# Performance work log

Measured on AMD Instinct MI355X. Metric: run time of the kernel, lower is better.

## Reference

```python
import jax, jax.numpy as jnp
import numpy as np

B, T, D, R = 4, 2048, 1024, 64  # batch, seq_len, hidden_dim, max_relative_position


def setup_inputs() -> dict:
    key = jax.random.key(0)
    ks = jax.random.split(key, 11)
    s = 1.0 / np.sqrt(D)

    def lin(k):
        return (jax.random.normal(k, (D, D), jnp.float32) * s)

    return {
        "repre": jax.random.normal(ks[0], (B, T, D), jnp.float32),
        "mask": jnp.ones((B, T, T), jnp.int32),  # 1 = valid position
        "st_Wq": lin(ks[1]), "st_bq": jnp.zeros((D,), jnp.float32),
        "st_Wk": lin(ks[2]), "st_bk": jnp.zeros((D,), jnp.float32),
        "st_rel": jax.random.normal(ks[3], (2 * R + 1, D), jnp.float32) * 0.02,
        "ed_Wq": lin(ks[4]), "ed_bq": jnp.zeros((D,), jnp.float32),
        "ed_Wk": lin(ks[5]), "ed_bk": jnp.zeros((D,), jnp.float32),
        "ed_rel": jax.random.normal(ks[6], (2 * R + 1, D), jnp.float32) * 0.02,
    }


def _attn_logits(x, Wq, bq, Wk, bk, rel, mask):
    # Single-head attention scores with relative-position key bias (OpenNMT style).
    d = x.shape[-1]
    q = (x @ Wq + bq) * (1.0 / jnp.sqrt(jnp.float32(d)))  # [B,T,D], pre-scaled query
    k = x @ Wk + bk                                        # [B,T,D]
    scores = jnp.einsum('btd,bsd->bts', q, k)              # [B,T,T] content scores
    Tn = x.shape[1]
    Rn = (rel.shape[0] - 1) // 2
    pos = jnp.arange(Tn)
    # relative position matrix: clip(j - i, -R, R) + R  -> [T,T] indices
    idx = jnp.clip(pos[None, :] - pos[:, None], -Rn, Rn) + Rn
    # q . rel_emb for every relative offset, then gather per (i,j):
    # equivalent to einsum('btd,tsd->bts', q, rel[idx]) without the [T,T,D] gather.
    qr = jnp.einsum('btd,rd->btr', q, rel)                 # [B,T,2R+1]
    scores = scores + qr[:, pos[:, None], idx]             # [B,T,T]
    return jnp.where(mask.astype(bool), scores, jnp.float32(-1e18))


def reference(repre, mask, st_Wq, st_bq, st_Wk, st_bk, st_rel,
              ed_Wq, ed_bq, ed_Wk, ed_bk, ed_rel):
    span_st_logits = _attn_logits(repre, st_Wq, st_bq, st_Wk, st_bk, st_rel, mask)
    span_ed_logits = _attn_logits(repre, ed_Wq, ed_bq, ed_Wk, ed_bk, ed_rel, mask)
    return (span_st_logits, span_ed_logits)
```

## Files before the change

kernel.cpp:

```cpp
#include <hip/hip_runtime.h>

constexpr int Bn = 4;
constexpr int Tn = 2048;
constexpr int Dn = 1024;
constexpr int Rn = 64;
constexpr int RELP = 256;
constexpr int QR_STRIDE = 132;

typedef __bf16 bf8 __attribute__((ext_vector_type(8)));
typedef float f32x4 __attribute__((ext_vector_type(4)));

__device__ __forceinline__ unsigned short f2bf(float f) {
    unsigned int u = __float_as_uint(f);
    u += 0x7fffu + ((u >> 16) & 1u);
    return (unsigned short)(u >> 16);
}

#define GLDS(g, l)                                                            \
    __builtin_amdgcn_global_load_lds(                                         \
        (const __attribute__((address_space(1))) void*)(g),                   \
        (__attribute__((address_space(3))) void*)(l), 16, 0, 0)

__device__ __forceinline__ void mfma_gemm_128(
    const unsigned short* __restrict__ Ab,
    const unsigned short* __restrict__ Bb,
    int K, f32x4 acc[4][4],
    unsigned short* As, unsigned short* Bs)
{
    const int tid = threadIdx.x;
    const int r0  = tid >> 2;
    const int c8  = (tid & 3) * 8;
    const int lane = tid & 63;
    const int w    = tid >> 6;
    const int wm = (w & 1) * 64, wn = (w >> 1) * 64;
    const int l15 = lane & 15, lq = lane >> 4;

    const int nt = K >> 5;

    GLDS(Ab + (size_t)r0 * K + c8,        As + r0 * 32 + c8);
    GLDS(Ab + ((size_t)r0 + 64) * K + c8, As + (r0 + 64) * 32 + c8);
    GLDS(Bb + (size_t)r0 * K + c8,        Bs + r0 * 32 + c8);
    GLDS(Bb + ((size_t)r0 + 64) * K + c8, Bs + (r0 + 64) * 32 + c8);
    __syncthreads();

    int cur = 0;
    for (int t = 0; t < nt; ++t) {
        if (t + 1 < nt) {
            const int k0 = (t + 1) << 5;
            const int nb = (cur ^ 1) * (128 * 32);
            GLDS(Ab + (size_t)r0 * K + k0 + c8,        As + nb + r0 * 32 + c8);
            GLDS(Ab + ((size_t)r0 + 64) * K + k0 + c8, As + nb + (r0 + 64) * 32 + c8);
            GLDS(Bb + (size_t)r0 * K + k0 + c8,        Bs + nb + r0 * 32 + c8);
            GLDS(Bb + ((size_t)r0 + 64) * K + k0 + c8, Bs + nb + (r0 + 64) * 32 + c8);
        }
        const int cb = cur * (128 * 32);
        bf8 a[4], b[4];
#pragma unroll
        for (int i = 0; i < 4; ++i) {
            a[i] = *(const bf8*)&As[cb + (wm + i * 16 + l15) * 32 + lq * 8];
            b[i] = *(const bf8*)&Bs[cb + (wn + i * 16 + l15) * 32 + lq * 8];
        }
#pragma unroll
        for (int i = 0; i < 4; ++i)
#pragma unroll
            for (int j = 0; j < 4; ++j)
                acc[i][j] = __builtin_amdgcn_mfma_f32_16x16x32_bf16(
                    a[i], b[j], acc[i][j], 0, 0, 0);
        __syncthreads();
        cur ^= 1;
    }
}

__global__ __launch_bounds__(256) void cvt_bf16(
    const float* __restrict__ in, unsigned short* __restrict__ out, int n4)
{
    int i = blockIdx.x * 256 + threadIdx.x;
    if (i < n4) {
        float4 v = ((const float4*)in)[i];
        ushort4 o;
        o.x = f2bf(v.x); o.y = f2bf(v.y); o.z = f2bf(v.z); o.w = f2bf(v.w);
        ((ushort4*)out)[i] = o;
    }
}

__global__ __launch_bounds__(256) void wt_transpose(
    const float* __restrict__ w0, const float* __restrict__ w1,
    const float* __restrict__ w2, const float* __restrict__ w3,
    unsigned short* __restrict__ WT)
{
    __shared__ float t[32][33];
    const int z = blockIdx.z;
    const float* W = z == 0 ? w0 : z == 1 ? w1 : z == 2 ? w2 : w3;
    const int x = blockIdx.x * 32 + threadIdx.x;
    const int y0 = blockIdx.y * 32;
#pragma unroll
    for (int j = 0; j < 32; j += 8)
        t[threadIdx.y + j][threadIdx.x] = W[(size_t)(y0 + threadIdx.y + j) * Dn + x];
    __syncthreads();
    unsigned short* o = WT + (size_t)z * Dn * Dn;
    const int n0 = blockIdx.x * 32;
#pragma unroll
    for (int j = 0; j < 32; j += 8)
        o[(size_t)(n0 + threadIdx.y + j) * Dn + y0 + threadIdx.x] =
            f2bf(t[threadIdx.x][threadIdx.y + j]);
}

__global__ __launch_bounds__(256) void rel_pad(
    const float* __restrict__ st_rel, const float* __restrict__ ed_rel,
    unsigned short* __restrict__ relb)
{
    const int z = blockIdx.y;
    const float* in = z ? ed_rel : st_rel;
    const int i4 = blockIdx.x * 256 + threadIdx.x;
    const int row = (i4 * 4) >> 10;
    const int col = (i4 * 4) & 1023;
    ushort4 o; o.x = 0; o.y = 0; o.z = 0; o.w = 0;
    if (row < 2 * Rn + 1) {
        float4 v = *(const float4*)(in + (size_t)row * 1024 + col);
        o.x = f2bf(v.x); o.y = f2bf(v.y); o.z = f2bf(v.z); o.w = f2bf(v.w);
    }
    ((ushort4*)(relb + (size_t)z * RELP * 1024))[i4] = o;
}

__global__ __launch_bounds__(256) void proj_gemm(
    const unsigned short* __restrict__ Xb, const unsigned short* __restrict__ Wb,
    const float* __restrict__ b0, const float* __restrict__ b1,
    const float* __restrict__ b2, const float* __restrict__ b3,
    unsigned short* __restrict__ outQK, float qscale)
{
    __shared__ unsigned short As[2 * 128 * 32], Bs[2 * 128 * 32];
    const int z = blockIdx.z;
    const float* bias = z == 0 ? b0 : z == 1 ? b1 : z == 2 ? b2 : b3;
    const float scale = (z & 1) ? 1.0f : qscale;

    const unsigned short* Ab = Xb + (size_t)blockIdx.x * 128 * Dn;
    const unsigned short* Bb = Wb + ((size_t)z * Dn + blockIdx.y * 128) * Dn;

    f32x4 zero = {0.f, 0.f, 0.f, 0.f};
    f32x4 acc[4][4];
#pragma unroll
    for (int i = 0; i < 4; ++i)
#pragma unroll
        for (int j = 0; j < 4; ++j) acc[i][j] = zero;

    mfma_gemm_128(Ab, Bb, Dn, acc, As, Bs);

    const int tid = threadIdx.x, lane = tid & 63, w = tid >> 6;
    const int wm = (w & 1) * 64, wn = (w >> 1) * 64;
    const int l15 = lane & 15, lq = lane >> 4;
    unsigned short* out = outQK + (size_t)z * (size_t)Bn * Tn * Dn;

#pragma unroll
    for (int ni = 0; ni < 4; ++ni) {
        const int col = blockIdx.y * 128 + wn + ni * 16 + l15;
        const float bv = bias[col];
#pragma unroll
        for (int mi = 0; mi < 4; ++mi) {
#pragma unroll
            for (int r = 0; r < 4; ++r) {
                const int row = blockIdx.x * 128 + wm + mi * 16 + lq * 4 + r;
                out[(size_t)row * Dn + col] = f2bf((acc[mi][ni][r] + bv) * scale);
            }
        }
    }
}

__global__ __launch_bounds__(256) void qr_gemm(
    const unsigned short* __restrict__ QKb, const unsigned short* __restrict__ relb,
    float* __restrict__ QR)
{
    __shared__ unsigned short As[2 * 128 * 32], Bs[2 * 128 * 32];
    const int z = blockIdx.z;
    const unsigned short* Ab = QKb + ((size_t)(z * 2) * Bn * Tn + blockIdx.x * 128) * Dn;
    const unsigned short* Bb = relb + ((size_t)z * RELP + blockIdx.y * 128) * Dn;

    f32x4 zero = {0.f, 0.f, 0.f, 0.f};
    f32x4 acc[4][4];
#pragma unroll
    for (int i = 0; i < 4; ++i)
#pragma unroll
        for (int j = 0; j < 4; ++j) acc[i][j] = zero;

    mfma_gemm_128(Ab, Bb, Dn, acc, As, Bs);

    const int tid = threadIdx.x, lane = tid & 63, w = tid >> 6;
    const int wm = (w & 1) * 64, wn = (w >> 1) * 64;
    const int l15 = lane & 15, lq = lane >> 4;
    float* out = QR + (size_t)z * (size_t)Bn * Tn * QR_STRIDE;

#pragma unroll
    for (int ni = 0; ni < 4; ++ni) {
        const int col = blockIdx.y * 128 + wn + ni * 16 + l15;
        if (col >= 2 * Rn + 1) continue;
#pragma unroll
        for (int mi = 0; mi < 4; ++mi) {
#pragma unroll
            for (int r = 0; r < 4; ++r) {
                const int row = blockIdx.x * 128 + wm + mi * 16 + lq * 4 + r;
                out[(size_t)row * QR_STRIDE + col] = acc[mi][ni][r];
            }
        }
    }
}

__global__ __launch_bounds__(256) void scores_gemm(
    const unsigned short* __restrict__ QKb, const float* __restrict__ QR,
    const int* __restrict__ mask, float* __restrict__ Out)
{
    __shared__ unsigned short As[2 * 128 * 32], Bs[2 * 128 * 32];
    const int z = blockIdx.z;
    const int side = z >> 2, bt = z & 3;

    const unsigned short* Ab =
        QKb + ((size_t)side * 2 * Bn * Tn + (size_t)bt * Tn + blockIdx.x * 128) * Dn;
    const unsigned short* Bb =
        QKb + (((size_t)side * 2 + 1) * Bn * Tn + (size_t)bt * Tn + blockIdx.y * 128) * Dn;
    const float* QRb = QR + ((size_t)side * Bn * Tn + (size_t)bt * Tn) * QR_STRIDE;
    const int* maskb = mask + (size_t)bt * Tn * Tn;
    float* outb = Out + ((size_t)side * Bn + bt) * (size_t)Tn * Tn;

    f32x4 zero = {0.f, 0.f, 0.f, 0.f};
    f32x4 acc[4][4];
#pragma unroll
    for (int i = 0; i < 4; ++i)
#pragma unroll
        for (int j = 0; j < 4; ++j) acc[i][j] = zero;

    mfma_gemm_128(Ab, Bb, Dn, acc, As, Bs);

    const int tid = threadIdx.x, lane = tid & 63, w = tid >> 6;
    const int wm = (w & 1) * 64, wn = (w >> 1) * 64;
    const int l15 = lane & 15, lq = lane >> 4;

#pragma unroll
    for (int mi = 0; mi < 4; ++mi) {
#pragma unroll
        for (int r = 0; r < 4; ++r) {
            const int i = blockIdx.x * 128 + wm + mi * 16 + lq * 4 + r;
            const float* qrow = QRb + (size_t)i * QR_STRIDE;
            const int* mrow = maskb + (size_t)i * Tn;
            float* orow = outb + (size_t)i * Tn;
#pragma unroll
            for (int ni = 0; ni < 4; ++ni) {
                const int j = blockIdx.y * 128 + wn + ni * 16 + l15;
                int d = j - i;
                d = d < -Rn ? -Rn : (d > Rn ? Rn : d);
                const float qv = qrow[d + Rn];
                orow[j] = mrow[j] ? acc[mi][ni][r] + qv : -1e18f;
            }
        }
    }
}

extern "C" void kernel_launch(void* const* d_in, const int* in_sizes, int n_in,
                              void* d_out, int out_size, void* d_ws, size_t ws_size,
                              hipStream_t stream) {
    const float* repre  = (const float*)d_in[0];
    const int*   mask   = (const int*)  d_in[1];
    const float* st_Wq  = (const float*)d_in[2];
    const float* st_bq  = (const float*)d_in[3];
    const float* st_Wk  = (const float*)d_in[4];
    const float* st_bk  = (const float*)d_in[5];
    const float* st_rel = (const float*)d_in[6];
    const float* ed_Wq  = (const float*)d_in[7];
    const float* ed_bq  = (const float*)d_in[8];
    const float* ed_Wk  = (const float*)d_in[9];
    const float* ed_bk  = (const float*)d_in[10];
    const float* ed_rel = (const float*)d_in[11];
    float* out = (float*)d_out;

    const size_t MT = (size_t)Bn * Tn;

    unsigned short* Xb   = (unsigned short*)d_ws;
    unsigned short* Wb   = Xb + MT * Dn;
    unsigned short* relb = Wb + (size_t)4 * Dn * Dn;
    unsigned short* QKb  = relb + (size_t)2 * RELP * Dn;
    float* QRbuf = (float*)(QKb + (size_t)4 * MT * Dn);

    const float qscale = 0.03125f;
    dim3 blk(256);

    {
        int n4 = (int)(MT * Dn / 4);
        cvt_bf16<<<dim3((n4 + 255) / 256), blk, 0, stream>>>(repre, Xb, n4);
        wt_transpose<<<dim3(32, 32, 4), dim3(32, 8), 0, stream>>>(
            st_Wq, st_Wk, ed_Wq, ed_Wk, Wb);
        rel_pad<<<dim3(RELP * Dn / 4 / 256, 2), blk, 0, stream>>>(st_rel, ed_rel, relb);
    }

    proj_gemm<<<dim3((int)MT / 128, Dn / 128, 4), blk, 0, stream>>>(
        Xb, Wb, st_bq, st_bk, ed_bq, ed_bk, QKb, qscale);

    qr_gemm<<<dim3((int)MT / 128, RELP / 128, 2), blk, 0, stream>>>(QKb, relb, QRbuf);

    scores_gemm<<<dim3(Tn / 128, Tn / 128, 8), blk, 0, stream>>>(QKb, QRbuf, mask, out);
}
```

Before: 557.8 us.

## Use 256x256 tiles with triple-buffered swizzled LDS pipeline for proj and score GEMMs

Replaces the 128x128 double-buffered GEMM core with a 256x256 tile per 512-thread block, an XOR-swizzled LDS layout, three-stage global_load_lds prefetch, and split MFMA phases under raised wave priority. Both the projection GEMM and the score GEMM now use it. The larger tiles cut global and LDS traffic per FLOP and the deeper pipeline is meant to hide load latency. The cost is more registers and LDS per block, fewer blocks in each grid, and hand-tuned waitcnt and barrier logic.

```diff
diff --git a/kernel.cpp b/kernel.cpp
--- a/kernel.cpp
+++ b/kernel.cpp
@@ -20,6 +20,100 @@
     __builtin_amdgcn_global_load_lds(                                         \
         (const __attribute__((address_space(1))) void*)(g),                   \
         (__attribute__((address_space(3))) void*)(l), 16, 0, 0)
+
+#define MFMA_BF16(a, b, c) __builtin_amdgcn_mfma_f32_16x16x32_bf16(a, b, c, 0, 0, 0)
+
+#define SBAR()                                                                \
+    do {                                                                      \
+        __builtin_amdgcn_sched_barrier(0);                                    \
+        __builtin_amdgcn_s_barrier();                                         \
+    } while (0)
+
+__device__ __forceinline__ void mfma_gemm_256_k32(
+    const unsigned short* __restrict__ Ab,
+    const unsigned short* __restrict__ Bb,
+    f32x4 (&acc)[8][4], unsigned short* As, unsigned short* Bs)
+{
+    const int tid  = threadIdx.x;
+    const int lane = tid & 63, wid = tid >> 6;
+    const int wr = wid >> 2, wc = wid & 3;
+    const int l15 = lane & 15, lq = lane >> 4;
+
+    const int pc = (((l15 & 1) << 2) | lq) ^ ((l15 >> 1) & 7);
+    const int lane_off = ((l15 >> 1) << 6) + (pc << 3);
+    const int aoff = wr * 4096 + lane_off;
+    const int boff = wc * 2048 + lane_off;
+
+    const int P0 = tid, P1 = tid + 512;
+    const int cr0 = P0 >> 3, cr1 = P1 >> 3;
+    const int c0 = cr0 * 8 + ((P0 & 7) ^ (cr0 & 7));
+    const int c1 = cr1 * 8 + ((P1 & 7) ^ (cr1 & 7));
+    const size_t g0 = (size_t)(c0 >> 2) * Dn + (size_t)((c0 & 3) << 3);
+    const size_t g1 = (size_t)(c1 >> 2) * Dn + (size_t)((c1 & 3) << 3);
+    const int d0 = P0 * 8, d1 = P1 * 8;
+
+#define STAGE(src, buf)                                                       \
+    do {                                                                      \
+        GLDS((src) + g0, (buf) + d0);                                         \
+        GLDS((src) + g1, (buf) + d1);                                         \
+    } while (0)
+
+    constexpr int NT = Dn / 32;
+
+    STAGE(Ab, As);
+    STAGE(Bb, Bs);
+    STAGE(Ab + 32, As + 8192);
+    STAGE(Bb + 32, Bs + 8192);
+    asm volatile("s_waitcnt vmcnt(4)" ::: "memory");
+    SBAR();
+
+    int bufi = 0;
+    bf8 a8[8], b4[4];
+#pragma unroll 1
+    for (int T = 0; T < NT; ++T) {
+        const int cb  = bufi << 13;
+        const int sb  = (bufi == 0 ? 2 : bufi - 1) << 13;
+        const bool st = T < NT - 2;
+        const unsigned short* At = Ab + (T + 2) * 32;
+        const unsigned short* Bt = Bb + (T + 2) * 32;
+
+#pragma unroll
+        for (int m = 0; m < 8; ++m)
+            a8[m] = *(const bf8*)&As[cb + aoff + m * 512];
+        b4[0] = *(const bf8*)&Bs[cb + boff];
+        b4[1] = *(const bf8*)&Bs[cb + boff + 512];
+        if (st) STAGE(At, As + sb);
+        SBAR();
+        __builtin_amdgcn_s_setprio(1);
+#pragma unroll
+        for (int m = 0; m < 8; ++m) {
+            acc[m][0] = MFMA_BF16(a8[m], b4[0], acc[m][0]);
+            acc[m][1] = MFMA_BF16(a8[m], b4[1], acc[m][1]);
+        }
+        __builtin_amdgcn_s_setprio(0);
+        SBAR();
+
+        b4[2] = *(const bf8*)&Bs[cb + boff + 1024];
+        b4[3] = *(const bf8*)&Bs[cb + boff + 1536];
+        if (st) STAGE(Bt, Bs + sb);
+        SBAR();
+        __builtin_amdgcn_s_setprio(1);
+#pragma unroll
+        for (int m = 0; m < 8; ++m) {
+            acc[m][2] = MFMA_BF16(a8[m], b4[2], acc[m][2]);
+            acc[m][3] = MFMA_BF16(a8[m], b4[3], acc[m][3]);
+        }
+        __builtin_amdgcn_s_setprio(0);
+        if (st) {
+            asm volatile("s_waitcnt vmcnt(4)" ::: "memory");
+        } else if (T == NT - 2) {
+            asm volatile("s_waitcnt vmcnt(0)" ::: "memory");
+        }
+        if (T < NT - 1) SBAR();
+        bufi = (bufi == 2) ? 0 : bufi + 1;
+    }
+#undef STAGE
+}
 
 __device__ __forceinline__ void mfma_gemm_128(
     const unsigned short* __restrict__ Ab,
@@ -53,19 +147,18 @@
             GLDS(Bb + (size_t)r0 * K + k0 + c8,        Bs + nb + r0 * 32 + c8);
             GLDS(Bb + ((size_t)r0 + 64) * K + k0 + c8, Bs + nb + (r0 + 64) * 32 + c8);
         }
-        const int cb = cur * (128 * 32);
+        const int cbuf = cur * (128 * 32);
         bf8 a[4], b[4];
 #pragma unroll
         for (int i = 0; i < 4; ++i) {
-            a[i] = *(const bf8*)&As[cb + (wm + i * 16 + l15) * 32 + lq * 8];
-            b[i] = *(const bf8*)&Bs[cb + (wn + i * 16 + l15) * 32 + lq * 8];
+            a[i] = *(const bf8*)&As[cbuf + (wm + i * 16 + l15) * 32 + lq * 8];
+            b[i] = *(const bf8*)&Bs[cbuf + (wn + i * 16 + l15) * 32 + lq * 8];
         }
 #pragma unroll
         for (int i = 0; i < 4; ++i)
 #pragma unroll
             for (int j = 0; j < 4; ++j)
-                acc[i][j] = __builtin_amdgcn_mfma_f32_16x16x32_bf16(
-                    a[i], b[j], acc[i][j], 0, 0, 0);
+                acc[i][j] = MFMA_BF16(a[i], b[j], acc[i][j]);
         __syncthreads();
         cur ^= 1;
     }
@@ -122,46 +215,47 @@
     ((ushort4*)(relb + (size_t)z * RELP * 1024))[i4] = o;
 }
 
-__global__ __launch_bounds__(256) void proj_gemm(
+__global__ __launch_bounds__(512, 2) void proj_gemm256(
     const unsigned short* __restrict__ Xb, const unsigned short* __restrict__ Wb,
     const float* __restrict__ b0, const float* __restrict__ b1,
     const float* __restrict__ b2, const float* __restrict__ b3,
     unsigned short* __restrict__ outQK, float qscale)
 {
-    __shared__ unsigned short As[2 * 128 * 32], Bs[2 * 128 * 32];
+    __shared__ unsigned short As[3 * 8192], Bs[3 * 8192];
     const int z = blockIdx.z;
     const float* bias = z == 0 ? b0 : z == 1 ? b1 : z == 2 ? b2 : b3;
     const float scale = (z & 1) ? 1.0f : qscale;
 
-    const unsigned short* Ab = Xb + (size_t)blockIdx.x * 128 * Dn;
-    const unsigned short* Bb = Wb + ((size_t)z * Dn + blockIdx.y * 128) * Dn;
+    const unsigned short* Ab = Xb + (size_t)blockIdx.x * 256 * Dn;
+    const unsigned short* Bb = Wb + ((size_t)z * Dn + blockIdx.y * 256) * Dn;
 
     f32x4 zero = {0.f, 0.f, 0.f, 0.f};
-    f32x4 acc[4][4];
-#pragma unroll
-    for (int i = 0; i < 4; ++i)
+    f32x4 acc[8][4];
+#pragma unroll
+    for (int i = 0; i < 8; ++i)
 #pragma unroll
         for (int j = 0; j < 4; ++j) acc[i][j] = zero;
 
-    mfma_gemm_128(Ab, Bb, Dn, acc, As, Bs);
-
-    const int tid = threadIdx.x, lane = tid & 63, w = tid >> 6;
-    const int wm = (w & 1) * 64, wn = (w >> 1) * 64;
+    mfma_gemm_256_k32(Ab, Bb, acc, As, Bs);
+
+    const int tid = threadIdx.x, lane = tid & 63, wid = tid >> 6;
+    const int wr = wid >> 2, wc = wid & 3;
     const int l15 = lane & 15, lq = lane >> 4;
     unsigned short* out = outQK + (size_t)z * (size_t)Bn * Tn * Dn;
+    const int row0 = blockIdx.x * 256 + wr * 128 + lq * 4;
+    const int col0 = blockIdx.y * 256 + wc * 64 + l15;
 
 #pragma unroll
     for (int ni = 0; ni < 4; ++ni) {
-        const int col = blockIdx.y * 128 + wn + ni * 16 + l15;
-        const float bv = bias[col];
-#pragma unroll
-        for (int mi = 0; mi < 4; ++mi) {
+        const int col = col0 + ni * 16;
+        const float bvv = bias[col];
+#pragma unroll
+        for (int mi = 0; mi < 8; ++mi)
 #pragma unroll
             for (int r = 0; r < 4; ++r) {
-                const int row = blockIdx.x * 128 + wm + mi * 16 + lq * 4 + r;
-                out[(size_t)row * Dn + col] = f2bf((acc[mi][ni][r] + bv) * scale);
+                const int row = row0 + mi * 16 + r;
+                out[(size_t)row * Dn + col] = f2bf((acc[mi][ni][r] + bvv) * scale);
             }
-        }
     }
 }
 
@@ -203,46 +297,48 @@
     }
 }
 
-__global__ __launch_bounds__(256) void scores_gemm(
+__global__ __launch_bounds__(512, 2) void scores_gemm256(
     const unsigned short* __restrict__ QKb, const float* __restrict__ QR,
     const int* __restrict__ mask, float* __restrict__ Out)
 {
-    __shared__ unsigned short As[2 * 128 * 32], Bs[2 * 128 * 32];
+    __shared__ unsigned short As[3 * 8192], Bs[3 * 8192];
     const int z = blockIdx.z;
     const int side = z >> 2, bt = z & 3;
 
     const unsigned short* Ab =
-        QKb + ((size_t)side * 2 * Bn * Tn + (size_t)bt * Tn + blockIdx.x * 128) * Dn;
+        QKb + ((size_t)side * 2 * Bn * Tn + (size_t)bt * Tn + blockIdx.x * 256) * Dn;
     const unsigned short* Bb =
-        QKb + (((size_t)side * 2 + 1) * Bn * Tn + (size_t)bt * Tn + blockIdx.y * 128) * Dn;
+        QKb + (((size_t)side * 2 + 1) * Bn * Tn + (size_t)bt * Tn + blockIdx.y * 256) * Dn;
     const float* QRb = QR + ((size_t)side * Bn * Tn + (size_t)bt * Tn) * QR_STRIDE;
     const int* maskb = mask + (size_t)bt * Tn * Tn;
     float* outb = Out + ((size_t)side * Bn + bt) * (size_t)Tn * Tn;
 
     f32x4 zero = {0.f, 0.f, 0.f, 0.f};
-    f32x4 acc[4][4];
-#pragma unroll
-    for (int i = 0; i < 4; ++i)
+    f32x4 acc[8][4];
+#pragma unroll
+    for (int i = 0; i < 8; ++i)
 #pragma unroll
         for (int j = 0; j < 4; ++j) acc[i][j] = zero;
 
-    mfma_gemm_128(Ab, Bb, Dn, acc, As, Bs);
-
-    const int tid = threadIdx.x, lane = tid & 63, w = tid >> 6;
-    const int wm = (w & 1) * 64, wn = (w >> 1) * 64;
-    const int l15 = lane & 15, lq = lane >> 4;
-
-#pragma unroll
-    for (int mi = 0; mi < 4; ++mi) {
+    mfma_gemm_256_k32(Ab, Bb, acc, As, Bs);
+
+    const int tid = threadIdx.x, lane = tid & 63, wid = tid >> 6;
+    const int wr = wid >> 2, wc = wid & 3;
+    const int l15 = lane & 15, lq = lane >> 4;
+    const int i0 = blockIdx.x * 256 + wr * 128 + lq * 4;
+    const int j0 = blockIdx.y * 256 + wc * 64 + l15;
+
+#pragma unroll
+    for (int mi = 0; mi < 8; ++mi) {
 #pragma unroll
         for (int r = 0; r < 4; ++r) {
-            const int i = blockIdx.x * 128 + wm + mi * 16 + lq * 4 + r;
+            const int i = i0 + mi * 16 + r;
             const float* qrow = QRb + (size_t)i * QR_STRIDE;
             const int* mrow = maskb + (size_t)i * Tn;
             float* orow = outb + (size_t)i * Tn;
 #pragma unroll
             for (int ni = 0; ni < 4; ++ni) {
-                const int j = blockIdx.y * 128 + wn + ni * 16 + l15;
+                const int j = j0 + ni * 16;
                 int d = j - i;
                 d = d < -Rn ? -Rn : (d > Rn ? Rn : d);
                 const float qv = qrow[d + Rn];
@@ -288,10 +384,11 @@
         rel_pad<<<dim3(RELP * Dn / 4 / 256, 2), blk, 0, stream>>>(st_rel, ed_rel, relb);
     }
 
-    proj_gemm<<<dim3((int)MT / 128, Dn / 128, 4), blk, 0, stream>>>(
+    proj_gemm256<<<dim3((int)MT / 256, Dn / 256, 4), dim3(512), 0, stream>>>(
         Xb, Wb, st_bq, st_bk, ed_bq, ed_bk, QKb, qscale);
 
     qr_gemm<<<dim3((int)MT / 128, RELP / 128, 2), blk, 0, stream>>>(QKb, relb, QRbuf);
 
-    scores_gemm<<<dim3(Tn / 128, Tn / 128, 8), blk, 0, stream>>>(QKb, QRbuf, mask, out);
-}
+    scores_gemm256<<<dim3(Tn / 256, Tn / 256, 8), dim3(512), 0, stream>>>(
+        QKb, QRbuf, mask, out);
+}
```

Result: slower. 569.7 us (+2.1%).
